# Kernel tuning notes

Hardware: AMD Instinct MI355X
Metric: run time of the kernel (lower is better)

## Reference

```python
import jax, jax.numpy as jnp
import numpy as np

L = 4          # n_layers
HID = 64       # hidden_channels
MODES = 16     # n_modes
HEADS = 4      # n_heads
NP_SP = 500    # spatial engram patterns
NP_FR = 200    # spectral engram patterns
ED = 8         # embed_dim
WS = 4         # spatial window size
PRIME = 31.0


def setup_inputs() -> dict:
    key = jax.random.key(0)
    ks = jax.random.split(key, 20)
    B, Cin, Cout, S = 16, 3, 1, 16384
    f = lambda k, sh: jax.random.normal(k, sh, dtype=jnp.float32) * 0.05
    ch = HID // HEADS
    return {
        "x": jax.random.normal(ks[0], (B, Cin, S), dtype=jnp.float32),
        "lift_W": f(ks[1], (Cin, HID)), "lift_b": f(ks[2], (HID,)),
        "proj_W": f(ks[3], (HID, Cout)), "proj_b": f(ks[4], (Cout,)),
        "sp_emb": f(ks[5], (L, NP_SP, ED)), "sp_W": f(ks[6], (L, ED, HID)), "sp_b": f(ks[7], (L, HID)),
        "fr_emb": f(ks[8], (L, NP_FR, ED)), "fr_W": f(ks[9], (L, ED, HID * MODES)), "fr_b": f(ks[10], (L, HID * MODES)),
        "g_W1": f(ks[11], (L, 3 * HID, 64)), "g_b1": f(ks[12], (L, 64)),
        "g_W2": f(ks[13], (L, 64, 3)), "g_b2": f(ks[14], (L, 3)),
        "mhf_Wr": f(ks[15], (L, HEADS, ch, ch, MODES)),
        "mhf_Wi": f(ks[16], (L, HEADS, ch, ch, MODES)),
    }


def _spatial_engram(x, emb, W, b):
    # x: [B, C, S] -> hash each replicate-padded window of size WS -> embedding gather -> linear
    B, C, S = x.shape
    pad = WS // 2
    xp = jnp.pad(x, ((0, 0), (0, 0), (pad, pad)), mode='edge')   # [B, C, S+WS]
    sC = xp.sum(axis=1)                                          # [B, S+WS]
    # window sum over WS consecutive positions (vectorized over all seq positions)
    wsum = sC[:, 0:S] + sC[:, 1:S + 1] + sC[:, 2:S + 2] + sC[:, 3:S + 3]  # [B, S]
    idx = (wsum * PRIME).astype(jnp.int32) % NP_SP               # truncate-toward-zero like torch .long()
    idx = jnp.clip(idx, 0, NP_SP - 1)
    e = emb[idx]                                                 # [B, S, ED] gather
    out = e @ W + b                                              # [B, S, C]
    return out.transpose(0, 2, 1)                                # [B, C, S]


def _spectral_engram(x, emb, W, b):
    B, C, S = x.shape
    xf = jnp.fft.rfft(x, axis=-1)                                # [B, C, F]
    mag = jnp.abs(xf[:, :, :MODES]).mean(axis=1)                 # [B, MODES]
    idx = ((mag * 1000.0).astype(jnp.int32)).sum(axis=1) % NP_FR # [B]
    e = emb[idx]                                                 # [B, ED]
    proj = (e @ W + b).reshape(B, C, MODES)
    full = jnp.zeros((B, C, xf.shape[-1]), dtype=xf.dtype).at[:, :, :MODES].set(proj.astype(xf.dtype))
    return jnp.fft.irfft(full, n=S, axis=-1)


def _mhf_spectral_conv(x, Wr, Wi):
    # multi-head Fourier spectral conv: per-head complex channel mixing on low modes
    B, C, S = x.shape
    ch = C // HEADS
    xf = jnp.fft.rfft(x, axis=-1)                                # [B, C, F]
    xh = xf[:, :, :MODES].reshape(B, HEADS, ch, MODES)           # [B, H, ch, M]
    Wc = Wr + 1j * Wi                                            # [H, ch, ch, M]
    of = jnp.einsum('bhim,hiom->bhom', xh, Wc).reshape(B, C, MODES)
    full = jnp.zeros((B, C, xf.shape[-1]), dtype=xf.dtype).at[:, :, :MODES].set(of)
    return jnp.fft.irfft(full, n=S, axis=-1)


def _gated_fusion(sp, mh, fr, W1, b1, W2, b2):
    g = jnp.concatenate([sp.mean(-1), mh.mean(-1), fr.mean(-1)], axis=-1)  # [B, 3C]
    h = jax.nn.relu(g @ W1 + b1)
    w = jax.nn.softmax(h @ W2 + b2, axis=-1)                     # [B, 3]
    return (w[:, 0, None, None] * sp + w[:, 1, None, None] * mh + w[:, 2, None, None] * fr)


def reference(x, lift_W, lift_b, proj_W, proj_b, sp_emb, sp_W, sp_b,
              fr_emb, fr_W, fr_b, g_W1, g_b1, g_W2, g_b2, mhf_Wr, mhf_Wi):
    # lifting: [B, Cin, S] -> [B, HID, S]
    h = jnp.einsum('bcs,cd->bds', x, lift_W) + lift_b[None, :, None]
    for i in range(L):
        sp = _spatial_engram(h, sp_emb[i], sp_W[i], sp_b[i])
        mh = _mhf_spectral_conv(h, mhf_Wr[i], mhf_Wi[i])
        fr = _spectral_engram(h, fr_emb[i], fr_W[i], fr_b[i])
        h = _gated_fusion(sp, mh, fr, g_W1[i], g_b1[i], g_W2[i], g_b2[i])
        h = jax.nn.gelu(h, approximate=False)  # torch F.gelu default = exact erf
    out = jnp.einsum('bcs,cd->bds', h, proj_W) + proj_b[None, :, None]
    return out
```

## Files before the change

kernel.cpp:

```cpp
#include <hip/hip_runtime.h>
#include <math.h>

#define B_ 16
#define CIN_ 3
#define HID_ 64
#define S_ 16384
#define MODES_ 16
#define HEADS_ 4
#define CH_ 16
#define ED_ 8
#define NPSP_ 500
#define NPFR_ 200
#define LAYERS_ 4
#define RECW_ 42

__device__ __forceinline__ double gelu_exact(double v) {
    double y = v * 0.70710678118654752440;
    double t = y * y;
    double p = -1.2290555301717926e-09;
    p = fma(p, t, 1.4807192815879218e-08);
    p = fma(p, t, -1.6365838718281893e-07);
    p = fma(p, t, 1.6462114365889246e-06);
    p = fma(p, t, -1.4925650358406251e-05);
    p = fma(p, t, 1.2055332981789664e-04);
    p = fma(p, t, -8.5483270234508528e-04);
    p = fma(p, t, 5.2239776254421878e-03);
    p = fma(p, t, -2.6866170645131252e-02);
    p = fma(p, t, 1.1283791670955126e-01);
    p = fma(p, t, -3.7612638903183752e-01);
    p = fma(p, t, 1.1283791670955126e+00);
    double er = y * p;
    if (t > 0.5000001) er = erf(y);
    return 0.5 * v * (1.0 + er);
}

__device__ __constant__ double KC_[16] = {1.0, 0.99518472667219688624,
    0.98078528040323044913, 0.95694033573220886494, 0.92387953251128675613,
    0.88192126434835502971, 0.83146961230254523708, 0.77301045336273696081,
    0.70710678118654752440, 0.63439328416364549822, 0.55557023301960222474,
    0.47139673682599764856, 0.38268343236508977173, 0.29028467725446236764,
    0.19509032201612826785, 0.09801714032956060199};
__device__ __constant__ double KS_[16] = {0.0, 0.09801714032956060199,
    0.19509032201612826785, 0.29028467725446236764, 0.38268343236508977173,
    0.47139673682599764856, 0.55557023301960222474, 0.63439328416364549822,
    0.70710678118654752440, 0.77301045336273696081, 0.83146961230254523708,
    0.88192126434835502971, 0.92387953251128675613, 0.95694033573220886494,
    0.98078528040323044913, 0.99518472667219688624};

__global__ __launch_bounds__(256) void k_lift(const float* __restrict__ x,
                                              const float* __restrict__ W,
                                              const float* __restrict__ bias,
                                              float* __restrict__ h,
                                              double* __restrict__ sC2) {
    int b = blockIdx.y;
    int s = blockIdx.x * 256 + threadIdx.x;
    const float* xb = x + (size_t)b * CIN_ * S_ + s;
    double x0 = (double)xb[0];
    double x1 = (double)xb[S_];
    double x2 = (double)xb[2 * S_];
    float* hb = h + (size_t)b * HID_ * S_ + s;
#pragma unroll
    for (int q = 0; q < 4; ++q) {
        double a = 0.0;
        for (int dd = 0; dd < 16; ++dd) {
            int d = q * 16 + dd;
            double v = x0 * (double)W[d];
            v = fma(x1, (double)W[HID_ + d], v);
            v = fma(x2, (double)W[2 * HID_ + d], v);
            v += (double)bias[d];
            hb[(size_t)d * S_] = (float)v;
            a += v;
        }
        sC2[(size_t)(q * B_ + b) * S_ + s] = a;
    }
}

__global__ __launch_bounds__(256) void k_hash(const double* __restrict__ sC2,
                                              const float* __restrict__ emb_l,
                                              int* __restrict__ idx,
                                              double* __restrict__ Eb) {
    int b = blockIdx.y;
    int s0 = blockIdx.x * 256;
    int t = threadIdx.x;
    __shared__ double sl[260];
    for (int j = t; j < 260; j += 256) {
        int p = s0 - 2 + j;
        p = p < 0 ? 0 : (p > S_ - 1 ? S_ - 1 : p);
        const double* sb = sC2 + (size_t)b * S_ + p;
        sl[j] = ((sb[0] + sb[(size_t)B_ * S_]) + sb[(size_t)2 * B_ * S_])
                + sb[(size_t)3 * B_ * S_];
    }
    __syncthreads();
    double wsum = ((sl[t] + sl[t + 1]) + sl[t + 2]) + sl[t + 3];
    int ti = (int)(wsum * 31.0);
    int id = ti % NPSP_;
    if (id < 0) id += NPSP_;
    idx[(size_t)b * S_ + s0 + t] = id;

    const float* er = emb_l + id * ED_;
    double ev[8];
#pragma unroll
    for (int k = 0; k < 8; k++) ev[k] = (double)er[k];

    int lane = t & 63, wv = t >> 6;
    __shared__ double red[4][8];
#pragma unroll
    for (int k = 0; k < 8; k++) {
        double v = ev[k];
        for (int off = 32; off > 0; off >>= 1) v += __shfl_down(v, off, 64);
        if (lane == 0) red[wv][k] = v;
    }
    __syncthreads();
    if (t < 8) {
        double v = red[0][t] + red[1][t] + red[2][t] + red[3][t];
        atomicAdd(&Eb[b * ED_ + t], v);
    }
}

__global__ __launch_bounds__(256, 2) void k_dft(const float* __restrict__ h,
                                                double* __restrict__ Xr,
                                                double* __restrict__ Xi) {
    int b = blockIdx.y;
    int c0 = blockIdx.x * 2;
    int t = threadIdx.x;
    const float* h0 = h + ((size_t)(b * HID_ + c0)) * S_ + t;
    const float* h1 = h0 + S_;

    double acc[64];
#pragma unroll
    for (int k = 0; k < 64; k++) acc[k] = 0.0;

    double cmv[16], smv[16];
    cmv[0] = 1.0; smv[0] = 0.0;
    cmv[1] = cospi((double)t / 8192.0);
    smv[1] = sinpi((double)t / 8192.0);
#pragma unroll
    for (int m = 2; m < 16; m++) {
        cmv[m] = cmv[m - 1] * cmv[1] - smv[m - 1] * smv[1];
        smv[m] = smv[m - 1] * cmv[1] + cmv[m - 1] * smv[1];
    }

    for (int k = 0; k < 16; k++) {
        int s = k << 8;
        double a0 = (double)h0[s];
        double b0 = (double)h0[s + 4096];
        double c0v = (double)h0[s + 8192];
        double d0 = (double)h0[s + 12288];
        double a1 = (double)h1[s];
        double b1 = (double)h1[s + 4096];
        double c1v = (double)h1[s + 8192];
        double d1 = (double)h1[s + 12288];

        double t10 = a0 + c0v, t20 = b0 + d0;
        double g00 = t10 + t20, g20 = t10 - t20;
        double ar0 = a0 - c0v, br0 = b0 - d0;
        double t11 = a1 + c1v, t21 = b1 + d1;
        double g01 = t11 + t21, g21 = t11 - t21;
        double ar1 = a1 - c1v, br1 = b1 - d1;

        acc[0] += g00;
        acc[32] += g01;
#pragma unroll
        for (int m = 1; m < 16; m++) {
            double c = cmv[m], s_ = smv[m];
            if ((m & 1) == 0) {
                double g0x = (m & 2) ? g20 : g00;
                double g1x = (m & 2) ? g21 : g01;
                acc[m]      = fma(g0x, c,  acc[m]);
                acc[16 + m] = fma(g0x, s_, acc[16 + m]);
                acc[32 + m] = fma(g1x, c,  acc[32 + m]);
                acc[48 + m] = fma(g1x, s_, acc[48 + m]);
            } else if ((m & 2) == 0) {
                acc[m]      = fma(ar0, c,  fma(-br0, s_, acc[m]));
                acc[16 + m] = fma(ar0, s_, fma( br0, c,  acc[16 + m]));
                acc[32 + m] = fma(ar1, c,  fma(-br1, s_, acc[32 + m]));
                acc[48 + m] = fma(ar1, s_, fma( br1, c,  acc[48 + m]));
            } else {
                acc[m]      = fma(ar0, c,  fma( br0, s_, acc[m]));
                acc[16 + m] = fma(ar0, s_, fma(-br0, c,  acc[16 + m]));
                acc[32 + m] = fma(ar1, c,  fma( br1, s_, acc[32 + m]));
                acc[48 + m] = fma(ar1, s_, fma(-br1, c,  acc[48 + m]));
            }
        }
#pragma unroll
        for (int m = 1; m < 16; m++) {
            double cn = cmv[m] * KC_[m] - smv[m] * KS_[m];
            double sn = smv[m] * KC_[m] + cmv[m] * KS_[m];
            cmv[m] = cn; smv[m] = sn;
        }
    }

    int lane = t & 63, wv = t >> 6;
    __shared__ double red[4][64];
#pragma unroll
    for (int k = 0; k < 64; k++) {
        double v = acc[k];
        for (int off = 32; off > 0; off >>= 1) v += __shfl_down(v, off, 64);
        if (lane == 0) red[wv][k] = v;
    }
    __syncthreads();
    if (t < 64) {
        double v = red[0][t] + red[1][t] + red[2][t] + red[3][t];
        int cc = t >> 5, im = (t >> 4) & 1, m = t & 15;
        size_t o = ((size_t)b * HID_ + c0 + cc) * MODES_ + m;
        if (im) Xi[o] = -v;
        else    Xr[o] = v;
    }
}

__global__ __launch_bounds__(256) void k_gate(const double* __restrict__ Xr,
                                              const double* __restrict__ Xi,
                                              const float* __restrict__ mWr,
                                              const float* __restrict__ mWi,
                                              const float* __restrict__ fr_emb_l,
                                              const float* __restrict__ fr_W_l,
                                              const float* __restrict__ fr_b_l,
                                              const double* __restrict__ Eb,
                                              const float* __restrict__ sp_W_l,
                                              const float* __restrict__ sp_b_l,
                                              const float* __restrict__ gW1,
                                              const float* __restrict__ gb1,
                                              const float* __restrict__ gW2,
                                              const float* __restrict__ gb2,
                                              double* __restrict__ RECg) {
    int b = blockIdx.x;
    int t = threadIdx.x;
    __shared__ double sXr[1024], sXi[1024];
    __shared__ double sMr[1024], sMi[1024], sP[1024];
    __shared__ double gg[192], h1s[64], sww[3];
    __shared__ int magI[MODES_];
    __shared__ int fidxS;

    for (int j = t; j < 1024; j += 256) {
        sXr[j] = Xr[(size_t)b * 1024 + j];
        sXi[j] = Xi[(size_t)b * 1024 + j];
    }
    __syncthreads();

    if (t < MODES_) {
        double acc = 0.0;
        for (int c = 0; c < HID_; c++) {
            double re = sXr[c * MODES_ + t];
            double im = sXi[c * MODES_ + t];
            acc += sqrt(re * re + im * im);
        }
        magI[t] = (int)(acc * (1.0 / 64.0) * 1000.0);
    }

    for (int u = t; u < 1024; u += 256) {
        int hh = u >> 8, rem = u & 255, o = rem >> 4, m = rem & 15;
        const float* wr = mWr + (size_t)hh * CH_ * CH_ * MODES_;
        const float* wi = mWi + (size_t)hh * CH_ * CH_ * MODES_;
        double aR = 0.0, aI = 0.0;
#pragma unroll 4
        for (int i = 0; i < CH_; i++) {
            double xrv = sXr[(hh * CH_ + i) * MODES_ + m];
            double xiv = sXi[(hh * CH_ + i) * MODES_ + m];
            double wrv = (double)wr[(i * CH_ + o) * MODES_ + m];
            double wiv = (double)wi[(i * CH_ + o) * MODES_ + m];
            aR += xrv * wrv - xiv * wiv;
            aI += xrv * wiv + xiv * wrv;
        }
        sMr[(hh * CH_ + o) * MODES_ + m] = aR;
        sMi[(hh * CH_ + o) * MODES_ + m] = aI;
    }
    __syncthreads();

    if (t == 0) {
        int ssum = 0;
        for (int m = 0; m < MODES_; m++) ssum += magI[m];
        int f = ssum % NPFR_;
        if (f < 0) f += NPFR_;
        fidxS = f;
    }
    __syncthreads();

    {
        const float* fe = fr_emb_l + fidxS * ED_;
        for (int u = t; u < 1024; u += 256) {
            double acc = 0.0;
            for (int e = 0; e < ED_; e++)
                acc += (double)fe[e] * (double)fr_W_l[e * 1024 + u];
            sP[u] = acc + (double)fr_b_l[u];
        }
    }
    __syncthreads();

    if (t < 64) {
        double a = 0.0;
        for (int e = 0; e < ED_; e++)
            a += Eb[b * ED_ + e] * (double)sp_W_l[e * 64 + t];
        gg[t]       = a * (1.0 / 16384.0) + (double)sp_b_l[t];
        gg[64 + t]  = sMr[t * MODES_] * (1.0 / 16384.0);
        gg[128 + t] = sP[t * MODES_] * (1.0 / 16384.0);
    }
    __syncthreads();
    if (t < 64) {
        double a = 0.0;
        for (int k = 0; k < 192; k++) a += gg[k] * (double)gW1[k * 64 + t];
        a += (double)gb1[t];
        h1s[t] = a > 0.0 ? a : 0.0;
    }
    __syncthreads();
    if (t == 0) {
        double l[3];
        for (int j = 0; j < 3; j++) {
            double a = 0.0;
            for (int k = 0; k < 64; k++) a += h1s[k] * (double)gW2[k * 3 + j];
            l[j] = a + (double)gb2[j];
        }
        double mx = fmax(l[0], fmax(l[1], l[2]));
        double e0 = exp(l[0] - mx), e1 = exp(l[1] - mx), e2 = exp(l[2] - mx);
        double sum = e0 + e1 + e2;
        sww[0] = e0 / sum; sww[1] = e1 / sum; sww[2] = e2 / sum;
    }
    __syncthreads();

    double w0s = sww[0], w1s = sww[1], w2s = sww[2];
    double* R = RECg + (size_t)b * HID_ * RECW_;
    for (int u = t; u < 1024; u += 256) {
        int c = u >> 4, m = u & 15;
        double km = (m == 0 ? 1.0 : 2.0) * (1.0 / 16384.0);
        R[c * RECW_ + 2 * m]     = km * (w1s * sMr[u] + w2s * sP[u]);
        R[c * RECW_ + 2 * m + 1] = (m == 0) ? 0.0 : -(km * w1s * sMi[u]);
    }
    for (int u = t; u < 512; u += 256) {
        int e = u >> 6, c = u & 63;
        R[c * RECW_ + 32 + e] = w0s * (double)sp_W_l[u];
    }
    if (t < 64) {
        R[t * RECW_ + 40] = w0s * (double)sp_b_l[t];
        R[t * RECW_ + 41] = 0.0;
    }
}

__global__ __launch_bounds__(256, 2) void k_recon(const int* __restrict__ idx,
                                                  const float* __restrict__ sp_emb_l,
                                                  const double* __restrict__ RECg,
                                                  float* __restrict__ h,
                                                  double* __restrict__ sC2) {
    int b = blockIdx.y;
    int cz = blockIdx.z;
    int cbase = cz * 16;
    int s0 = blockIdx.x * 256 + threadIdx.x;
    int t = threadIdx.x;
    __shared__ float semb[NPSP_ * 9];
    for (int j4 = t; j4 < NPSP_ * 2; j4 += 256) {
        float4 v = reinterpret_cast<const float4*>(sp_emb_l)[j4];
        int r = j4 >> 1, e0 = (j4 & 1) * 4;
        semb[r * 9 + e0]     = v.x;
        semb[r * 9 + e0 + 1] = v.y;
        semb[r * 9 + e0 + 2] = v.z;
        semb[r * 9 + e0 + 3] = v.w;
    }
    __syncthreads();

    int id0 = idx[(size_t)b * S_ + s0];
    int id1 = idx[(size_t)b * S_ + s0 + 4096];
    int id2 = idx[(size_t)b * S_ + s0 + 8192];
    int id3 = idx[(size_t)b * S_ + s0 + 12288];
    double e0v[8], e1v[8], e2v[8], e3v[8];
#pragma unroll
    for (int k = 0; k < 8; k++) {
        e0v[k] = (double)semb[id0 * 9 + k];
        e1v[k] = (double)semb[id1 * 9 + k];
        e2v[k] = (double)semb[id2 * 9 + k];
        e3v[k] = (double)semb[id3 * 9 + k];
    }

    double cb = cospi((double)s0 / 8192.0);
    double sb = sinpi((double)s0 / 8192.0);
    double cm[16], sm[16];
    cm[0] = 1.0; sm[0] = 0.0;
    cm[1] = cb;  sm[1] = sb;
#pragma unroll
    for (int m = 2; m < 16; m++) {
        cm[m] = cm[m - 1] * cb - sm[m - 1] * sb;
        sm[m] = sm[m - 1] * cb + cm[m - 1] * sb;
    }

    const double* Rb = RECg + ((size_t)b * HID_ + cbase) * RECW_;
    float* hb = h + (size_t)b * HID_ * S_ + (size_t)cbase * S_;
    double cs0 = 0.0, cs1 = 0.0, cs2 = 0.0, cs3 = 0.0;
#pragma unroll 1
    for (int c = 0; c < 16; c++) {
        const double2* r2 = (const double2*)(Rb + (size_t)c * RECW_);
        double base = Rb[(size_t)c * RECW_ + 40];
        double p0 = base, p1 = base, p2 = base, p3 = base;
#pragma unroll
        for (int k = 0; k < 4; k++) {
            double2 w = r2[16 + k];
            p0 = fma(e0v[2 * k], w.x, p0); p0 = fma(e0v[2 * k + 1], w.y, p0);
            p1 = fma(e1v[2 * k], w.x, p1); p1 = fma(e1v[2 * k + 1], w.y, p1);
            p2 = fma(e2v[2 * k], w.x, p2); p2 = fma(e2v[2 * k + 1], w.y, p2);
            p3 = fma(e3v[2 * k], w.x, p3); p3 = fma(e3v[2 * k + 1], w.y, p3);
        }
        double PA = 0.0, PB = 0.0, PC = 0.0, PD = 0.0, QB = 0.0, QD = 0.0;
#pragma unroll
        for (int mm = 0; mm < 16; mm += 4) {
            double2 q0 = r2[mm], q1 = r2[mm + 1], q2 = r2[mm + 2], q3 = r2[mm + 3];
            PA = fma(q0.x, cm[mm], PA);     PA = fma(q0.y, sm[mm], PA);
            PB = fma(q1.x, cm[mm + 1], PB); PB = fma(q1.y, sm[mm + 1], PB);
            QB = fma(q1.y, cm[mm + 1], QB); QB = fma(-q1.x, sm[mm + 1], QB);
            PC = fma(q2.x, cm[mm + 2], PC); PC = fma(q2.y, sm[mm + 2], PC);
            PD = fma(q3.x, cm[mm + 3], PD); PD = fma(q3.y, sm[mm + 3], PD);
            QD = fma(q3.y, cm[mm + 3], QD); QD = fma(-q3.x, sm[mm + 3], QD);
        }
        double u0 = PA + PC, u1 = PA - PC;
        double w0 = PB + PD, qd = QB - QD;
        double g0 = gelu_exact(p0 + (u0 + w0));
        double g1 = gelu_exact(p1 + (u1 + qd));
        double g2 = gelu_exact(p2 + (u0 - w0));
        double g3 = gelu_exact(p3 + (u1 - qd));
        hb[(size_t)c * S_ + s0]         = (float)g0;
        hb[(size_t)c * S_ + s0 + 4096]  = (float)g1;
        hb[(size_t)c * S_ + s0 + 8192]  = (float)g2;
        hb[(size_t)c * S_ + s0 + 12288] = (float)g3;
        cs0 += g0; cs1 += g1; cs2 += g2; cs3 += g3;
    }
    double* sc = sC2 + (size_t)(cz * B_ + b) * S_;
    sc[s0]         = cs0;
    sc[s0 + 4096]  = cs1;
    sc[s0 + 8192]  = cs2;
    sc[s0 + 12288] = cs3;
}

__global__ __launch_bounds__(256) void k_proj(const float* __restrict__ h,
                                              const float* __restrict__ pW,
                                              const float* __restrict__ pb,
                                              float* __restrict__ out) {
    int b = blockIdx.y;
    int s = blockIdx.x * 256 + threadIdx.x;
    const float* hb = h + (size_t)b * HID_ * S_ + s;
    double acc = 0.0;
    for (int d = 0; d < HID_; d++)
        acc += (double)hb[(size_t)d * S_] * (double)pW[d];
    out[(size_t)b * S_ + s] = (float)(acc + (double)pb[0]);
}

extern "C" void kernel_launch(void* const* d_in, const int* in_sizes, int n_in,
                              void* d_out, int out_size, void* d_ws, size_t ws_size,
                              hipStream_t stream) {
    const float* x      = (const float*)d_in[0];
    const float* lift_W = (const float*)d_in[1];
    const float* lift_b = (const float*)d_in[2];
    const float* proj_W = (const float*)d_in[3];
    const float* proj_b = (const float*)d_in[4];
    const float* sp_emb = (const float*)d_in[5];
    const float* sp_W   = (const float*)d_in[6];
    const float* sp_b   = (const float*)d_in[7];
    const float* fr_emb = (const float*)d_in[8];
    const float* fr_W   = (const float*)d_in[9];
    const float* fr_b   = (const float*)d_in[10];
    const float* g_W1   = (const float*)d_in[11];
    const float* g_b1   = (const float*)d_in[12];
    const float* g_W2   = (const float*)d_in[13];
    const float* g_b2   = (const float*)d_in[14];
    const float* mhf_Wr = (const float*)d_in[15];
    const float* mhf_Wi = (const float*)d_in[16];

    char* ws = (char*)d_ws;
    float* h    = (float*)ws;   ws += (size_t)B_ * HID_ * S_ * 4;
    double* sC2 = (double*)ws;  ws += (size_t)4 * B_ * S_ * 8;
    int* idx    = (int*)ws;     ws += (size_t)B_ * S_ * 4;
    double* Xr  = (double*)ws;  ws += (size_t)B_ * HID_ * MODES_ * 8;
    double* Xi  = (double*)ws;  ws += (size_t)B_ * HID_ * MODES_ * 8;
    double* REC = (double*)ws;  ws += (size_t)B_ * HID_ * RECW_ * 8;
    double* Eb  = (double*)ws;  ws += (size_t)LAYERS_ * B_ * ED_ * 8;

    hipMemsetAsync(Eb, 0, (size_t)LAYERS_ * B_ * ED_ * 8, stream);

    dim3 blk(256);
    k_lift<<<dim3(S_ / 256, B_), blk, 0, stream>>>(x, lift_W, lift_b, h, sC2);

    for (int lay = 0; lay < LAYERS_; ++lay) {
        k_hash<<<dim3(S_ / 256, B_), blk, 0, stream>>>(
            sC2, sp_emb + (size_t)lay * NPSP_ * ED_, idx, Eb + (size_t)lay * B_ * ED_);
        k_dft<<<dim3(HID_ / 2, B_), blk, 0, stream>>>(h, Xr, Xi);
        k_gate<<<dim3(B_), blk, 0, stream>>>(
            Xr, Xi,
            mhf_Wr + (size_t)lay * HEADS_ * CH_ * CH_ * MODES_,
            mhf_Wi + (size_t)lay * HEADS_ * CH_ * CH_ * MODES_,
            fr_emb + (size_t)lay * NPFR_ * ED_,
            fr_W + (size_t)lay * ED_ * HID_ * MODES_,
            fr_b + (size_t)lay * HID_ * MODES_,
            Eb + (size_t)lay * B_ * ED_,
            sp_W + (size_t)lay * ED_ * HID_,
            sp_b + (size_t)lay * HID_,
            g_W1 + (size_t)lay * 192 * 64,
            g_b1 + (size_t)lay * 64,
            g_W2 + (size_t)lay * 64 * 3,
            g_b2 + (size_t)lay * 3,
            REC);
        k_recon<<<dim3(S_ / 1024, B_, 4), blk, 0, stream>>>(
            idx, sp_emb + (size_t)lay * NPSP_ * ED_, REC, h, sC2);
    }

    k_proj<<<dim3(S_ / 256, B_), blk, 0, stream>>>(h, proj_W, proj_b, (float*)d_out);
}
```

Before: 579.4 us.

## Precompute spatial engram emb@W tables and gather per channel in recon

Adds a kernel that computes, once per call, a per-layer table of each embedding pattern projected onto each hidden channel (emb @ sp_W), stored as float. The recon kernel then loads the 16-channel slice of this table into shared memory and does a single gather plus fma per channel, instead of an 8-term dot product per position per channel. The gate weight w0 is applied at use time, and the REC record shrinks from 42 to 34 doubles. This costs a larger shared-memory footprint (32KB per block), which may lower occupancy, and rounds the projected values to float, which changes precision slightly.

```diff
diff --git a/kernel.cpp b/kernel.cpp
--- a/kernel.cpp
+++ b/kernel.cpp
@@ -12,7 +12,7 @@
 #define NPSP_ 500
 #define NPFR_ 200
 #define LAYERS_ 4
-#define RECW_ 42
+#define RECW_ 34
 
 __device__ __forceinline__ double gelu_exact(double v) {
     double y = v * 0.70710678118654752440;
@@ -46,6 +46,20 @@
     0.70710678118654752440, 0.77301045336273696081, 0.83146961230254523708,
     0.88192126434835502971, 0.92387953251128675613, 0.95694033573220886494,
     0.98078528040323044913, 0.99518472667219688624};
+
+__global__ __launch_bounds__(256) void k_sptab(const float* __restrict__ sp_emb,
+                                               const float* __restrict__ sp_W,
+                                               float* __restrict__ T0f) {
+    int lay = blockIdx.y;
+    int tid = blockIdx.x * 256 + threadIdx.x;
+    int c = tid & 63, id = tid >> 6;
+    const float* e = sp_emb + (size_t)lay * NPSP_ * ED_ + (size_t)id * ED_;
+    const float* w = sp_W + (size_t)lay * ED_ * HID_ + c;
+    double a = 0.0;
+#pragma unroll
+    for (int k = 0; k < ED_; k++) a = fma((double)e[k], (double)w[k * HID_], a);
+    T0f[((size_t)lay * HID_ + c) * NPSP_ + id] = (float)a;
+}
 
 __global__ __launch_bounds__(256) void k_lift(const float* __restrict__ x,
                                               const float* __restrict__ W,
@@ -324,18 +338,14 @@
         R[c * RECW_ + 2 * m]     = km * (w1s * sMr[u] + w2s * sP[u]);
         R[c * RECW_ + 2 * m + 1] = (m == 0) ? 0.0 : -(km * w1s * sMi[u]);
     }
-    for (int u = t; u < 512; u += 256) {
-        int e = u >> 6, c = u & 63;
-        R[c * RECW_ + 32 + e] = w0s * (double)sp_W_l[u];
-    }
     if (t < 64) {
-        R[t * RECW_ + 40] = w0s * (double)sp_b_l[t];
-        R[t * RECW_ + 41] = 0.0;
+        R[t * RECW_ + 32] = w0s * (double)sp_b_l[t];
+        R[t * RECW_ + 33] = w0s;
     }
 }
 
 __global__ __launch_bounds__(256, 2) void k_recon(const int* __restrict__ idx,
-                                                  const float* __restrict__ sp_emb_l,
+                                                  const float* __restrict__ T0f_l,
                                                   const double* __restrict__ RECg,
                                                   float* __restrict__ h,
                                                   double* __restrict__ sC2) {
@@ -344,14 +354,11 @@
     int cbase = cz * 16;
     int s0 = blockIdx.x * 256 + threadIdx.x;
     int t = threadIdx.x;
-    __shared__ float semb[NPSP_ * 9];
-    for (int j4 = t; j4 < NPSP_ * 2; j4 += 256) {
-        float4 v = reinterpret_cast<const float4*>(sp_emb_l)[j4];
-        int r = j4 >> 1, e0 = (j4 & 1) * 4;
-        semb[r * 9 + e0]     = v.x;
-        semb[r * 9 + e0 + 1] = v.y;
-        semb[r * 9 + e0 + 2] = v.z;
-        semb[r * 9 + e0 + 3] = v.w;
+    __shared__ __align__(16) float sT[16 * NPSP_];
+    {
+        const float4* src = reinterpret_cast<const float4*>(T0f_l + (size_t)cbase * NPSP_);
+        float4* dst = reinterpret_cast<float4*>(sT);
+        for (int j = t; j < 16 * NPSP_ / 4; j += 256) dst[j] = src[j];
     }
     __syncthreads();
 
@@ -359,14 +366,6 @@
     int id1 = idx[(size_t)b * S_ + s0 + 4096];
     int id2 = idx[(size_t)b * S_ + s0 + 8192];
     int id3 = idx[(size_t)b * S_ + s0 + 12288];
-    double e0v[8], e1v[8], e2v[8], e3v[8];
-#pragma unroll
-    for (int k = 0; k < 8; k++) {
-        e0v[k] = (double)semb[id0 * 9 + k];
-        e1v[k] = (double)semb[id1 * 9 + k];
-        e2v[k] = (double)semb[id2 * 9 + k];
-        e3v[k] = (double)semb[id3 * 9 + k];
-    }
 
     double cb = cospi((double)s0 / 8192.0);
     double sb = sinpi((double)s0 / 8192.0);
@@ -380,21 +379,18 @@
     }
 
     const double* Rb = RECg + ((size_t)b * HID_ + cbase) * RECW_;
+    double w0g = Rb[33];
     float* hb = h + (size_t)b * HID_ * S_ + (size_t)cbase * S_;
     double cs0 = 0.0, cs1 = 0.0, cs2 = 0.0, cs3 = 0.0;
 #pragma unroll 1
     for (int c = 0; c < 16; c++) {
         const double2* r2 = (const double2*)(Rb + (size_t)c * RECW_);
-        double base = Rb[(size_t)c * RECW_ + 40];
-        double p0 = base, p1 = base, p2 = base, p3 = base;
-#pragma unroll
-        for (int k = 0; k < 4; k++) {
-            double2 w = r2[16 + k];
-            p0 = fma(e0v[2 * k], w.x, p0); p0 = fma(e0v[2 * k + 1], w.y, p0);
-            p1 = fma(e1v[2 * k], w.x, p1); p1 = fma(e1v[2 * k + 1], w.y, p1);
-            p2 = fma(e2v[2 * k], w.x, p2); p2 = fma(e2v[2 * k + 1], w.y, p2);
-            p3 = fma(e3v[2 * k], w.x, p3); p3 = fma(e3v[2 * k + 1], w.y, p3);
-        }
+        const float* tc = sT + c * NPSP_;
+        double bias = Rb[(size_t)c * RECW_ + 32];
+        double p0 = fma(w0g, (double)tc[id0], bias);
+        double p1 = fma(w0g, (double)tc[id1], bias);
+        double p2 = fma(w0g, (double)tc[id2], bias);
+        double p3 = fma(w0g, (double)tc[id3], bias);
         double PA = 0.0, PB = 0.0, PC = 0.0, PD = 0.0, QB = 0.0, QD = 0.0;
 #pragma unroll
         for (int mm = 0; mm < 16; mm += 4) {
@@ -467,10 +463,12 @@
     double* Xi  = (double*)ws;  ws += (size_t)B_ * HID_ * MODES_ * 8;
     double* REC = (double*)ws;  ws += (size_t)B_ * HID_ * RECW_ * 8;
     double* Eb  = (double*)ws;  ws += (size_t)LAYERS_ * B_ * ED_ * 8;
+    float* T0f  = (float*)ws;   ws += (size_t)LAYERS_ * HID_ * NPSP_ * 4;
 
     hipMemsetAsync(Eb, 0, (size_t)LAYERS_ * B_ * ED_ * 8, stream);
 
     dim3 blk(256);
+    k_sptab<<<dim3(NPSP_ * HID_ / 256, LAYERS_), blk, 0, stream>>>(sp_emb, sp_W, T0f);
     k_lift<<<dim3(S_ / 256, B_), blk, 0, stream>>>(x, lift_W, lift_b, h, sC2);
 
     for (int lay = 0; lay < LAYERS_; ++lay) {
@@ -493,7 +491,7 @@
             g_b2 + (size_t)lay * 3,
             REC);
         k_recon<<<dim3(S_ / 1024, B_, 4), blk, 0, stream>>>(
-            idx, sp_emb + (size_t)lay * NPSP_ * ED_, REC, h, sC2);
+            idx, T0f + (size_t)lay * HID_ * NPSP_, REC, h, sC2);
     }
 
     k_proj<<<dim3(S_ / 256, B_), blk, 0, stream>>>(h, proj_W, proj_b, (float*)d_out);
```

New measurement: 559.8 us. 1.04x faster.
